# Performance work log

Hardware: AMD Instinct MI355X
Metric: run time of the kernel (lower is better)

## Reference

```python
import jax, jax.numpy as jnp
import numpy as np

NUM_HEADS = 4
NUM_GROUPS = 32
EPS = 1e-6


def group_norm(x, gamma, beta):
    # x: [b, c, h, w]
    b, c, h, w = x.shape
    xg = x.reshape(b, NUM_GROUPS, c // NUM_GROUPS, h, w)
    mu = xg.mean(axis=(2, 3, 4), keepdims=True)
    var = xg.var(axis=(2, 3, 4), keepdims=True)
    xn = ((xg - mu) * jax.lax.rsqrt(var + EPS)).reshape(b, c, h, w)
    return xn * gamma[None, :, None, None] + beta[None, :, None, None]


def conv1x1(x, W, b):
    # 1x1 conv == per-pixel channel matmul. W: [out_c, in_c], b: [out_c]
    return jnp.einsum('bchw,oc->bohw', x, W) + b[None, :, None, None]


def setup_inputs() -> dict:
    key = jax.random.key(0)
    ks = jax.random.split(key, 8)
    c = 256
    b, h, w = 1, 64, 64
    s = 1.0 / np.sqrt(c)
    return {
        'x_kv': jax.random.normal(ks[0], (b, c, h, w), dtype=jnp.float32),
        'gn_gamma': jnp.ones((c,), dtype=jnp.float32),
        'gn_beta': jnp.zeros((c,), dtype=jnp.float32),
        'Wq': jax.random.normal(ks[1], (c, c), dtype=jnp.float32) * s,
        'bq': jnp.zeros((c,), dtype=jnp.float32),
        'Wk': jax.random.normal(ks[2], (c, c), dtype=jnp.float32) * s,
        'bk': jnp.zeros((c,), dtype=jnp.float32),
        'Wv': jax.random.normal(ks[3], (c, c), dtype=jnp.float32) * s,
        'bv': jnp.zeros((c,), dtype=jnp.float32),
        'Wp': jax.random.normal(ks[4], (c, c), dtype=jnp.float32) * s,
        'bp': jnp.zeros((c,), dtype=jnp.float32),
    }


def reference(x_kv, gn_gamma, gn_beta, Wq, bq, Wk, bk, Wv, bv, Wp, bp):
    b, c, h, w = x_kv.shape
    hd = c // NUM_HEADS
    n = h * w

    h_norm = group_norm(x_kv, gn_gamma, gn_beta)  # self-attn: same norm for q,k,v

    q = conv1x1(h_norm, Wq, bq).reshape(b, NUM_HEADS, hd, n).transpose(0, 1, 3, 2)  # [b,H,n,hd]
    k = conv1x1(h_norm, Wk, bk).reshape(b, NUM_HEADS, hd, n)                        # [b,H,hd,n]
    v = conv1x1(h_norm, Wv, bv).reshape(b, NUM_HEADS, hd, n).transpose(0, 1, 3, 2)  # [b,H,n,hd]

    scores = jnp.einsum('bhnd,bhdm->bhnm', q, k) * (hd ** -0.5)  # [b,H,n,n]
    attn = jax.nn.softmax(scores, axis=-1)
    out = jnp.einsum('bhnm,bhmd->bhnd', attn, v)  # [b,H,n,hd]

    # Faithful to torch: permute(0,2,1,3).contiguous().view(b,c,h,w)
    out = out.transpose(0, 2, 1, 3).reshape(b, c, h, w)
    return x_kv + conv1x1(out, Wp, bp)
```

## Files before the change

### kernel.cpp

```cpp
#include <hip/hip_runtime.h>
#include <hip/hip_bf16.h>

#define NPIX 4096
#define CCH  256
#define HD   64
#define GSIZE 32768

#define QSCALE 0.18033688f

typedef __bf16 bf16x8 __attribute__((ext_vector_type(8)));
typedef __bf16 bf16x4 __attribute__((ext_vector_type(4)));
typedef __bf16 bf16x2 __attribute__((ext_vector_type(2)));
typedef float  f32x4  __attribute__((ext_vector_type(4)));
typedef unsigned int uint32x4 __attribute__((ext_vector_type(4)));

#define XPITCH 264

#if __has_builtin(__builtin_amdgcn_exp2f)
#define EXP2(x) __builtin_amdgcn_exp2f(x)
#else
#define EXP2(x) __expf((x) * 0.6931471805599453f)
#endif


__device__ __forceinline__ unsigned pack_bf16x2(float lo, float hi)
{
    bf16x2 v;
    v[0] = (__bf16)lo;
    v[1] = (__bf16)hi;
    return __builtin_bit_cast(unsigned, v);
}

__global__ __launch_bounds__(256) void stats_wconv(
    const float* __restrict__ X,
    const float* __restrict__ Wq, const float* __restrict__ Wk,
    const float* __restrict__ Wv, const float* __restrict__ Wp,
    float* __restrict__ psum, float* __restrict__ pssq, __bf16* __restrict__ Wb)
{
    const int bid = blockIdx.x, t = threadIdx.x;
    if (bid < 256) {
        const float* base = X + bid * 4096;
        float sum = 0.f, ssq = 0.f;
        #pragma unroll
        for (int k = 0; k < 4; ++k) {
            float4 v = *(const float4*)(base + t * 4 + k * 1024);
            sum += v.x + v.y + v.z + v.w;
            ssq += v.x * v.x + v.y * v.y + v.z * v.z + v.w * v.w;
        }
        #pragma unroll
        for (int off = 1; off < 64; off <<= 1) {
            sum += __shfl_xor(sum, off);
            ssq += __shfl_xor(ssq, off);
        }
        __shared__ float red[2][4];
        const int wv = t >> 6;
        if ((t & 63) == 0) { red[0][wv] = sum; red[1][wv] = ssq; }
        __syncthreads();
        if (t == 0) {
            psum[bid] = red[0][0] + red[0][1] + red[0][2] + red[0][3];
            pssq[bid] = red[1][0] + red[1][1] + red[1][2] + red[1][3];
        }
    } else {
        const int j0 = (bid - 256) * 4096 + t * 16;
        const int m  = j0 >> 16;
        const float* W = (m == 0) ? Wq : (m == 1) ? Wk : (m == 2) ? Wv : Wp;
        const float sc = (m == 0) ? QSCALE : 1.f;
        const int off = j0 & 65535;
        #pragma unroll
        for (int k = 0; k < 4; ++k) {
            float4 v = *(const float4*)(W + off + k * 4);
            bf16x4 o;
            o[0] = (__bf16)(v.x * sc); o[1] = (__bf16)(v.y * sc);
            o[2] = (__bf16)(v.z * sc); o[3] = (__bf16)(v.w * sc);
            *(bf16x4*)(Wb + m * 65536 + off + k * 4) = o;
        }
    }
}

__global__ __launch_bounds__(256) void gn_qkv(
    const float* __restrict__ X, const float* __restrict__ gamma,
    const float* __restrict__ beta,
    const float* __restrict__ psum, const float* __restrict__ pssq,
    const __bf16* __restrict__ Wb,
    const float* __restrict__ bq, const float* __restrict__ bk,
    const float* __restrict__ bv,
    __bf16* __restrict__ Qb, __bf16* __restrict__ Kb, __bf16* __restrict__ Vb)
{
    __shared__ __bf16 tile[64 * XPITCH];
    __shared__ float al[256], bl[256];

    const int t = threadIdx.x, lane = t & 63, wave = t >> 6;
    const int l16 = lane & 15, quad = lane >> 4;
    const int p0 = blockIdx.x * 64;
    const int z = blockIdx.y >> 1, och = blockIdx.y & 1;

    {
        const int g = t >> 3;
        float s = 0.f, q = 0.f;
        #pragma unroll
        for (int j = 0; j < 8; ++j) { s += psum[g * 8 + j]; q += pssq[g * 8 + j]; }
        const float mu  = s * (1.f / GSIZE);
        const float var = q * (1.f / GSIZE) - mu * mu;
        const float a = gamma[t] * rsqrtf(var + 1e-6f);
        al[t] = a;
        bl[t] = beta[t] - mu * a;
    }
    __syncthreads();

    #pragma unroll 4
    for (int i = 0; i < 16; ++i) {
        const int c4 = wave * 64 + i * 4;
        f32x4 a4 = *(const f32x4*)(al + c4);
        f32x4 b4 = *(const f32x4*)(bl + c4);
        bf16x4 pk;
        pk[0] = (__bf16)(X[(c4 + 0) * NPIX + p0 + lane] * a4[0] + b4[0]);
        pk[1] = (__bf16)(X[(c4 + 1) * NPIX + p0 + lane] * a4[1] + b4[1]);
        pk[2] = (__bf16)(X[(c4 + 2) * NPIX + p0 + lane] * a4[2] + b4[2]);
        pk[3] = (__bf16)(X[(c4 + 3) * NPIX + p0 + lane] * a4[3] + b4[3]);
        *(bf16x4*)(tile + lane * XPITCH + c4) = pk;
    }
    __syncthreads();

    const int pw = wave * 16;
    bf16x8 xf[8];
    #pragma unroll
    for (int kc = 0; kc < 8; ++kc)
        xf[kc] = *(const bf16x8*)(tile + (pw + l16) * XPITCH + kc * 32 + quad * 8);

    const __bf16* Wz = Wb + z * 65536;
    const float* bias = (z == 0) ? bq : (z == 1) ? bk : bv;

    if (z < 2) {
        const float qs = (z == 0) ? QSCALE : 1.f;
        __bf16* dst = (z == 0) ? Qb : Kb;
        #pragma unroll
        for (int grp = 0; grp < 2; ++grp) {
            f32x4 acc[4] = {};
            #pragma unroll
            for (int kc = 0; kc < 8; ++kc) {
                #pragma unroll
                for (int u = 0; u < 4; ++u) {
                    bf16x8 wf = *(const bf16x8*)(Wz + (och * 128 + (grp * 4 + u) * 16 + l16) * CCH + kc * 32 + quad * 8);
                    acc[u] = __builtin_amdgcn_mfma_f32_16x16x32_bf16(wf, xf[kc], acc[u], 0, 0, 0);
                }
            }
            #pragma unroll
            for (int u = 0; u < 4; ++u) {
                const int ot = och * 8 + grp * 4 + u;
                f32x4 bz = *(const f32x4*)(bias + och * 128 + (grp * 4 + u) * 16 + quad * 4);
                bf16x4 o;
                o[0] = (__bf16)(acc[u][0] + bz[0] * qs);
                o[1] = (__bf16)(acc[u][1] + bz[1] * qs);
                o[2] = (__bf16)(acc[u][2] + bz[2] * qs);
                o[3] = (__bf16)(acc[u][3] + bz[3] * qs);
                const int head = ot >> 2, dloc = (ot & 3) * 16 + quad * 4;
                *(bf16x4*)(dst + head * (NPIX * HD) + (p0 + pw + l16) * HD + dloc) = o;
            }
        }
    } else {
        #pragma unroll
        for (int grp = 0; grp < 2; ++grp) {
            f32x4 acc[4] = {};
            #pragma unroll
            for (int kc = 0; kc < 8; ++kc) {
                #pragma unroll
                for (int u = 0; u < 4; ++u) {
                    bf16x8 wf = *(const bf16x8*)(Wz + (och * 128 + (grp * 4 + u) * 16 + l16) * CCH + kc * 32 + quad * 8);
                    acc[u] = __builtin_amdgcn_mfma_f32_16x16x32_bf16(xf[kc], wf, acc[u], 0, 0, 0);
                }
            }
            #pragma unroll
            for (int u = 0; u < 4; ++u) {
                const int oc = och * 128 + (grp * 4 + u) * 16 + l16;
                const float bz = bias[oc];
                bf16x4 o;
                o[0] = (__bf16)(acc[u][0] + bz); o[1] = (__bf16)(acc[u][1] + bz);
                o[2] = (__bf16)(acc[u][2] + bz); o[3] = (__bf16)(acc[u][3] + bz);
                *(bf16x4*)(Vb + oc * NPIX + p0 + pw + quad * 4) = o;
            }
        }
    }
}

__global__ __launch_bounds__(256, 1) void attn_mfma(
    const __bf16* __restrict__ Qb, const __bf16* __restrict__ Kb,
    const __bf16* __restrict__ Vb, __bf16* __restrict__ Sb)
{
    __shared__ __align__(16) float co[4 * 64 * 68];
    __shared__ float cl[4 * 64];

    const int t = threadIdx.x, lane = t & 63, wave = t >> 6;
    const int l16 = lane & 15, quad = lane >> 4;

    const int bid  = blockIdx.x;
    const int head = (bid & 7) >> 1;
    const int qt   = ((bid >> 3) << 1) | (bid & 1);
    const int p0   = qt * 64;

    const __bf16* Qh = Qb + head * (NPIX * HD);
    const __bf16* Kh = Kb + head * (NPIX * HD) + (wave * 32 + l16) * HD + quad * 8;
    const __bf16* Vh = Vb + head * (HD * NPIX) + l16 * NPIX + wave * 32 + quad * 8;

    bf16x8 qf[4][2];
    #pragma unroll
    for (int rt = 0; rt < 4; ++rt) {
        const __bf16* qp = Qh + (p0 + rt * 16 + l16) * HD + quad * 8;
        qf[rt][0] = *(const bf16x8*)(qp);
        qf[rt][1] = *(const bf16x8*)(qp + 32);
    }

    bf16x8 ones;
    #pragma unroll
    for (int j = 0; j < 8; ++j) ones[j] = (__bf16)1.0f;

    f32x4 l_acc[4] = {};
    f32x4 o_acc[4][4] = {};

    auto ldKV = [&](int it,
                    bf16x8& k0, bf16x8& k1, bf16x8& k2, bf16x8& k3,
                    bf16x8& v0, bf16x8& v1, bf16x8& v2, bf16x8& v3) {
        const __bf16* kp = Kh + it * (128 * HD);
        k0 = *(const bf16x8*)(kp);
        k1 = *(const bf16x8*)(kp + 32);
        k2 = *(const bf16x8*)(kp + 16 * HD);
        k3 = *(const bf16x8*)(kp + 16 * HD + 32);
        const __bf16* vp = Vh + it * 128;
        v0 = *(const bf16x8*)(vp);
        v1 = *(const bf16x8*)(vp + 16 * NPIX);
        v2 = *(const bf16x8*)(vp + 32 * NPIX);
        v3 = *(const bf16x8*)(vp + 48 * NPIX);
    };

    auto step = [&](bf16x8 k0, bf16x8 k1, bf16x8 k2, bf16x8 k3,
                    bf16x8 v0, bf16x8 v1, bf16x8 v2, bf16x8 v3) {
        f32x4 st0[4] = {}, st1[4] = {};
        #pragma unroll
        for (int rt = 0; rt < 4; ++rt) {
            st0[rt] = __builtin_amdgcn_mfma_f32_16x16x32_bf16(k0, qf[rt][0], st0[rt], 0, 0, 0);
            st0[rt] = __builtin_amdgcn_mfma_f32_16x16x32_bf16(k1, qf[rt][1], st0[rt], 0, 0, 0);
            st1[rt] = __builtin_amdgcn_mfma_f32_16x16x32_bf16(k2, qf[rt][0], st1[rt], 0, 0, 0);
            st1[rt] = __builtin_amdgcn_mfma_f32_16x16x32_bf16(k3, qf[rt][1], st1[rt], 0, 0, 0);
        }
        #pragma unroll
        for (int rt = 0; rt < 4; ++rt) {
            unsigned a0 = pack_bf16x2(EXP2(st0[rt][0]), EXP2(st0[rt][1]));
            unsigned a1 = pack_bf16x2(EXP2(st0[rt][2]), EXP2(st0[rt][3]));
            unsigned b0 = pack_bf16x2(EXP2(st1[rt][0]), EXP2(st1[rt][1]));
            unsigned b1 = pack_bf16x2(EXP2(st1[rt][2]), EXP2(st1[rt][3]));
            asm("v_permlane32_swap_b32 %0, %1" : "+v"(a0), "+v"(b0));
            asm("v_permlane32_swap_b32 %0, %1" : "+v"(a1), "+v"(b1));
            asm("v_permlane16_swap_b32 %0, %1" : "+v"(a0), "+v"(b0));
            asm("v_permlane16_swap_b32 %0, %1" : "+v"(a1), "+v"(b1));
            uint32x4 w;
            w[0] = a0; w[1] = a1; w[2] = b0; w[3] = b1;
            const bf16x8 bp = __builtin_bit_cast(bf16x8, w);
            l_acc[rt] = __builtin_amdgcn_mfma_f32_16x16x32_bf16(ones, bp, l_acc[rt], 0, 0, 0);
            o_acc[0][rt] = __builtin_amdgcn_mfma_f32_16x16x32_bf16(v0, bp, o_acc[0][rt], 0, 0, 0);
            o_acc[1][rt] = __builtin_amdgcn_mfma_f32_16x16x32_bf16(v1, bp, o_acc[1][rt], 0, 0, 0);
            o_acc[2][rt] = __builtin_amdgcn_mfma_f32_16x16x32_bf16(v2, bp, o_acc[2][rt], 0, 0, 0);
            o_acc[3][rt] = __builtin_amdgcn_mfma_f32_16x16x32_bf16(v3, bp, o_acc[3][rt], 0, 0, 0);
        }
    };

    bf16x8 ka0, ka1, ka2, ka3, va0, va1, va2, va3;
    bf16x8 kb0, kb1, kb2, kb3, vb0, vb1, vb2, vb3;
    bf16x8 kc0, kc1, kc2, kc3, vc0, vc1, vc2, vc3;

    ldKV(0, ka0, ka1, ka2, ka3, va0, va1, va2, va3);
    ldKV(1, kb0, kb1, kb2, kb3, vb0, vb1, vb2, vb3);

    #pragma unroll 1
    for (int it = 0; it < 30; it += 3) {
        ldKV(it + 2, kc0, kc1, kc2, kc3, vc0, vc1, vc2, vc3);
        step(ka0, ka1, ka2, ka3, va0, va1, va2, va3);
        ldKV(it + 3, ka0, ka1, ka2, ka3, va0, va1, va2, va3);
        step(kb0, kb1, kb2, kb3, vb0, vb1, vb2, vb3);
        ldKV(it + 4, kb0, kb1, kb2, kb3, vb0, vb1, vb2, vb3);
        step(kc0, kc1, kc2, kc3, vc0, vc1, vc2, vc3);
    }
    step(ka0, ka1, ka2, ka3, va0, va1, va2, va3);
    step(kb0, kb1, kb2, kb3, vb0, vb1, vb2, vb3);

    #pragma unroll
    for (int dt = 0; dt < 4; ++dt)
        #pragma unroll
        for (int rt = 0; rt < 4; ++rt)
            *(f32x4*)(co + wave * 4352 + (rt * 16 + l16) * 68 + dt * 16 + quad * 4) = o_acc[dt][rt];
    if (quad == 0) {
        #pragma unroll
        for (int rt = 0; rt < 4; ++rt)
            cl[wave * 64 + rt * 16 + l16] = l_acc[rt][0];
    }
    __syncthreads();

    {
        const int row = t >> 2, dc = (t & 3) * 16;
        const float l = cl[row] + cl[64 + row] + cl[128 + row] + cl[192 + row];
        const float inv = 1.f / l;
        f32x4 s[4];
        #pragma unroll
        for (int j = 0; j < 4; ++j) {
            s[j] = f32x4{0.f, 0.f, 0.f, 0.f};
            #pragma unroll
            for (int w = 0; w < 4; ++w)
                s[j] += *(const f32x4*)(co + w * 4352 + row * 68 + dc + j * 4);
        }
        bf16x8 o1, o2;
        #pragma unroll
        for (int j = 0; j < 4; ++j) {
            o1[j]     = (__bf16)(s[0][j] * inv);
            o1[j + 4] = (__bf16)(s[1][j] * inv);
            o2[j]     = (__bf16)(s[2][j] * inv);
            o2[j + 4] = (__bf16)(s[3][j] * inv);
        }
        __bf16* dst = Sb + (p0 + row) * CCH + head * HD + dc;
        *(bf16x8*)(dst)     = o1;
        *(bf16x8*)(dst + 8) = o2;
    }
}

__global__ __launch_bounds__(256) void gemm_proj(
    const __bf16* __restrict__ Sb, const __bf16* __restrict__ Wpb,
    const float* __restrict__ bias, const float* __restrict__ X,
    float* __restrict__ Out)
{
    __shared__ __bf16 Bs[32 * XPITCH];

    const int t = threadIdx.x, lane = t & 63, wave = t >> 6;
    const int l16 = lane & 15, quad = lane >> 4;
    const int p0  = blockIdx.x * 32;
    const int och = blockIdx.y;

    #pragma unroll
    for (int pg = 0; pg < 4; ++pg) {
        bf16x8 v = *(const bf16x8*)(Sb + t * NPIX + p0 + pg * 8);
        #pragma unroll
        for (int j = 0; j < 8; ++j)
            Bs[(pg * 8 + j) * XPITCH + t] = v[j];
    }
    __syncthreads();

    const int pixset = wave & 1, ocset = wave >> 1;
    bf16x8 af[8];
    #pragma unroll
    for (int kc = 0; kc < 8; ++kc)
        af[kc] = *(const bf16x8*)(Bs + (pixset * 16 + l16) * XPITCH + kc * 32 + quad * 8);

    #pragma unroll
    for (int u = 0; u < 4; ++u) {
        f32x4 acc = {};
        const int oc_t = och * 128 + ocset * 64 + u * 16;
        #pragma unroll
        for (int kc = 0; kc < 8; ++kc) {
            bf16x8 wf = *(const bf16x8*)(Wpb + (oc_t + l16) * CCH + kc * 32 + quad * 8);
            acc = __builtin_amdgcn_mfma_f32_16x16x32_bf16(af[kc], wf, acc, 0, 0, 0);
        }
        const int oc  = oc_t + l16;
        const int pix = p0 + pixset * 16 + quad * 4;
        const float bz = bias[oc];
        f32x4 r4 = *(const f32x4*)(X + oc * NPIX + pix);
        f32x4 y;
        y[0] = acc[0] + bz + r4[0];
        y[1] = acc[1] + bz + r4[1];
        y[2] = acc[2] + bz + r4[2];
        y[3] = acc[3] + bz + r4[3];
        *(f32x4*)(Out + oc * NPIX + pix) = y;
    }
}

extern "C" void kernel_launch(void* const* d_in, const int* in_sizes, int n_in,
                              void* d_out, int out_size, void* d_ws, size_t ws_size,
                              hipStream_t stream)
{
    const float* x     = (const float*)d_in[0];
    const float* gamma = (const float*)d_in[1];
    const float* beta  = (const float*)d_in[2];
    const float* Wq    = (const float*)d_in[3];
    const float* bq    = (const float*)d_in[4];
    const float* Wk    = (const float*)d_in[5];
    const float* bk    = (const float*)d_in[6];
    const float* Wv    = (const float*)d_in[7];
    const float* bv    = (const float*)d_in[8];
    const float* Wp    = (const float*)d_in[9];
    const float* bp    = (const float*)d_in[10];
    float* out = (float*)d_out;

    char* ws = (char*)d_ws;
    float*  psum = (float*)(ws);
    float*  pssq = (float*)(ws + 1024);
    __bf16* Wb   = (__bf16*)(ws + 65536);
    __bf16* Qb   = (__bf16*)(ws + (1 << 20));
    __bf16* Kb   = (__bf16*)(ws + (3 << 20));
    __bf16* Vb   = (__bf16*)(ws + (5 << 20));
    __bf16* Sb   = (__bf16*)(ws + (7 << 20));

    stats_wconv<<<320, 256, 0, stream>>>(x, Wq, Wk, Wv, Wp, psum, pssq, Wb);

    dim3 gq(64, 6);
    gn_qkv<<<gq, 256, 0, stream>>>(x, gamma, beta, psum, pssq, Wb,
                                   bq, bk, bv, Qb, Kb, Vb);

    attn_mfma<<<256, 256, 0, stream>>>(Qb, Kb, Vb, Sb);

    dim3 gp(128, 2);
    gemm_proj<<<gp, 256, 0, stream>>>(Sb, Wb + 3 * 65536, bp, x, out);
}
```

Baseline: 140.9 us.

## Split attention over key halves with 128-row query tiles, merge in projection

The attention kernel now processes 128 query rows per block instead of 64, and each block covers only half of the keys. It writes unnormalized fp32 partial outputs and row sums to workspace. The projection GEMM then sums the two halves and normalizes them while staging its input. This doubles K/V reuse per load and keeps the grid at 256 blocks, at the cost of more registers, a larger LDS footprint, and extra fp32 partial traffic through global memory.

```diff
diff --git a/kernel.cpp b/kernel.cpp
--- a/kernel.cpp
+++ b/kernel.cpp
@@ -182,28 +182,31 @@
     }
 }
 
-__global__ __launch_bounds__(256, 1) void attn_mfma(
+__global__ __launch_bounds__(256, 1) void attn_partial(
     const __bf16* __restrict__ Qb, const __bf16* __restrict__ Kb,
-    const __bf16* __restrict__ Vb, __bf16* __restrict__ Sb)
-{
-    __shared__ __align__(16) float co[4 * 64 * 68];
-    __shared__ float cl[4 * 64];
+    const __bf16* __restrict__ Vb, float* __restrict__ Op,
+    float* __restrict__ Lp)
+{
+    __shared__ __align__(16) float co[4 * 128 * 68];
+    __shared__ float cl[4 * 128];
 
     const int t = threadIdx.x, lane = t & 63, wave = t >> 6;
     const int l16 = lane & 15, quad = lane >> 4;
 
     const int bid  = blockIdx.x;
     const int head = (bid & 7) >> 1;
-    const int qt   = ((bid >> 3) << 1) | (bid & 1);
-    const int p0   = qt * 64;
+    const int half = bid & 1;
+    const int qt   = bid >> 3;
+    const int p0   = qt * 128;
+    const int kt0  = half * 16;
 
     const __bf16* Qh = Qb + head * (NPIX * HD);
     const __bf16* Kh = Kb + head * (NPIX * HD) + (wave * 32 + l16) * HD + quad * 8;
     const __bf16* Vh = Vb + head * (HD * NPIX) + l16 * NPIX + wave * 32 + quad * 8;
 
-    bf16x8 qf[4][2];
-    #pragma unroll
-    for (int rt = 0; rt < 4; ++rt) {
+    bf16x8 qf[8][2];
+    #pragma unroll
+    for (int rt = 0; rt < 8; ++rt) {
         const __bf16* qp = Qh + (p0 + rt * 16 + l16) * HD + quad * 8;
         qf[rt][0] = *(const bf16x8*)(qp);
         qf[rt][1] = *(const bf16x8*)(qp + 32);
@@ -213,8 +216,8 @@
     #pragma unroll
     for (int j = 0; j < 8; ++j) ones[j] = (__bf16)1.0f;
 
-    f32x4 l_acc[4] = {};
-    f32x4 o_acc[4][4] = {};
+    f32x4 l_acc[8] = {};
+    f32x4 o_acc[4][8] = {};
 
     auto ldKV = [&](int it,
                     bf16x8& k0, bf16x8& k1, bf16x8& k2, bf16x8& k3,
@@ -233,94 +236,89 @@
 
     auto step = [&](bf16x8 k0, bf16x8 k1, bf16x8 k2, bf16x8 k3,
                     bf16x8 v0, bf16x8 v1, bf16x8 v2, bf16x8 v3) {
-        f32x4 st0[4] = {}, st1[4] = {};
-        #pragma unroll
-        for (int rt = 0; rt < 4; ++rt) {
-            st0[rt] = __builtin_amdgcn_mfma_f32_16x16x32_bf16(k0, qf[rt][0], st0[rt], 0, 0, 0);
-            st0[rt] = __builtin_amdgcn_mfma_f32_16x16x32_bf16(k1, qf[rt][1], st0[rt], 0, 0, 0);
-            st1[rt] = __builtin_amdgcn_mfma_f32_16x16x32_bf16(k2, qf[rt][0], st1[rt], 0, 0, 0);
-            st1[rt] = __builtin_amdgcn_mfma_f32_16x16x32_bf16(k3, qf[rt][1], st1[rt], 0, 0, 0);
-        }
-        #pragma unroll
-        for (int rt = 0; rt < 4; ++rt) {
-            unsigned a0 = pack_bf16x2(EXP2(st0[rt][0]), EXP2(st0[rt][1]));
-            unsigned a1 = pack_bf16x2(EXP2(st0[rt][2]), EXP2(st0[rt][3]));
-            unsigned b0 = pack_bf16x2(EXP2(st1[rt][0]), EXP2(st1[rt][1]));
-            unsigned b1 = pack_bf16x2(EXP2(st1[rt][2]), EXP2(st1[rt][3]));
-            asm("v_permlane32_swap_b32 %0, %1" : "+v"(a0), "+v"(b0));
-            asm("v_permlane32_swap_b32 %0, %1" : "+v"(a1), "+v"(b1));
-            asm("v_permlane16_swap_b32 %0, %1" : "+v"(a0), "+v"(b0));
-            asm("v_permlane16_swap_b32 %0, %1" : "+v"(a1), "+v"(b1));
-            uint32x4 w;
-            w[0] = a0; w[1] = a1; w[2] = b0; w[3] = b1;
-            const bf16x8 bp = __builtin_bit_cast(bf16x8, w);
-            l_acc[rt] = __builtin_amdgcn_mfma_f32_16x16x32_bf16(ones, bp, l_acc[rt], 0, 0, 0);
-            o_acc[0][rt] = __builtin_amdgcn_mfma_f32_16x16x32_bf16(v0, bp, o_acc[0][rt], 0, 0, 0);
-            o_acc[1][rt] = __builtin_amdgcn_mfma_f32_16x16x32_bf16(v1, bp, o_acc[1][rt], 0, 0, 0);
-            o_acc[2][rt] = __builtin_amdgcn_mfma_f32_16x16x32_bf16(v2, bp, o_acc[2][rt], 0, 0, 0);
-            o_acc[3][rt] = __builtin_amdgcn_mfma_f32_16x16x32_bf16(v3, bp, o_acc[3][rt], 0, 0, 0);
+        #pragma unroll
+        for (int rtb = 0; rtb < 2; ++rtb) {
+            f32x4 st0[4] = {}, st1[4] = {};
+            #pragma unroll
+            for (int rt = 0; rt < 4; ++rt) {
+                const int r = rtb * 4 + rt;
+                st0[rt] = __builtin_amdgcn_mfma_f32_16x16x32_bf16(k0, qf[r][0], st0[rt], 0, 0, 0);
+                st0[rt] = __builtin_amdgcn_mfma_f32_16x16x32_bf16(k1, qf[r][1], st0[rt], 0, 0, 0);
+                st1[rt] = __builtin_amdgcn_mfma_f32_16x16x32_bf16(k2, qf[r][0], st1[rt], 0, 0, 0);
+                st1[rt] = __builtin_amdgcn_mfma_f32_16x16x32_bf16(k3, qf[r][1], st1[rt], 0, 0, 0);
+            }
+            #pragma unroll
+            for (int rt = 0; rt < 4; ++rt) {
+                const int r = rtb * 4 + rt;
+                unsigned a0 = pack_bf16x2(EXP2(st0[rt][0]), EXP2(st0[rt][1]));
+                unsigned a1 = pack_bf16x2(EXP2(st0[rt][2]), EXP2(st0[rt][3]));
+                unsigned b0 = pack_bf16x2(EXP2(st1[rt][0]), EXP2(st1[rt][1]));
+                unsigned b1 = pack_bf16x2(EXP2(st1[rt][2]), EXP2(st1[rt][3]));
+                asm("v_permlane32_swap_b32 %0, %1" : "+v"(a0), "+v"(b0));
+                asm("v_permlane32_swap_b32 %0, %1" : "+v"(a1), "+v"(b1));
+                asm("v_permlane16_swap_b32 %0, %1" : "+v"(a0), "+v"(b0));
+                asm("v_permlane16_swap_b32 %0, %1" : "+v"(a1), "+v"(b1));
+                uint32x4 w;
+                w[0] = a0; w[1] = a1; w[2] = b0; w[3] = b1;
+                const bf16x8 bp = __builtin_bit_cast(bf16x8, w);
+                l_acc[r] = __builtin_amdgcn_mfma_f32_16x16x32_bf16(ones, bp, l_acc[r], 0, 0, 0);
+                o_acc[0][r] = __builtin_amdgcn_mfma_f32_16x16x32_bf16(v0, bp, o_acc[0][r], 0, 0, 0);
+                o_acc[1][r] = __builtin_amdgcn_mfma_f32_16x16x32_bf16(v1, bp, o_acc[1][r], 0, 0, 0);
+                o_acc[2][r] = __builtin_amdgcn_mfma_f32_16x16x32_bf16(v2, bp, o_acc[2][r], 0, 0, 0);
+                o_acc[3][r] = __builtin_amdgcn_mfma_f32_16x16x32_bf16(v3, bp, o_acc[3][r], 0, 0, 0);
+            }
         }
     };
 
     bf16x8 ka0, ka1, ka2, ka3, va0, va1, va2, va3;
     bf16x8 kb0, kb1, kb2, kb3, vb0, vb1, vb2, vb3;
-    bf16x8 kc0, kc1, kc2, kc3, vc0, vc1, vc2, vc3;
-
-    ldKV(0, ka0, ka1, ka2, ka3, va0, va1, va2, va3);
-    ldKV(1, kb0, kb1, kb2, kb3, vb0, vb1, vb2, vb3);
-
+
+    ldKV(kt0, ka0, ka1, ka2, ka3, va0, va1, va2, va3);
     #pragma unroll 1
-    for (int it = 0; it < 30; it += 3) {
-        ldKV(it + 2, kc0, kc1, kc2, kc3, vc0, vc1, vc2, vc3);
+    for (int it = 0; it < 16; it += 2) {
+        ldKV(kt0 + it + 1, kb0, kb1, kb2, kb3, vb0, vb1, vb2, vb3);
         step(ka0, ka1, ka2, ka3, va0, va1, va2, va3);
-        ldKV(it + 3, ka0, ka1, ka2, ka3, va0, va1, va2, va3);
+        if (it + 2 < 16)
+            ldKV(kt0 + it + 2, ka0, ka1, ka2, ka3, va0, va1, va2, va3);
         step(kb0, kb1, kb2, kb3, vb0, vb1, vb2, vb3);
-        ldKV(it + 4, kb0, kb1, kb2, kb3, vb0, vb1, vb2, vb3);
-        step(kc0, kc1, kc2, kc3, vc0, vc1, vc2, vc3);
-    }
-    step(ka0, ka1, ka2, ka3, va0, va1, va2, va3);
-    step(kb0, kb1, kb2, kb3, vb0, vb1, vb2, vb3);
+    }
 
     #pragma unroll
     for (int dt = 0; dt < 4; ++dt)
         #pragma unroll
-        for (int rt = 0; rt < 4; ++rt)
-            *(f32x4*)(co + wave * 4352 + (rt * 16 + l16) * 68 + dt * 16 + quad * 4) = o_acc[dt][rt];
+        for (int rt = 0; rt < 8; ++rt)
+            *(f32x4*)(co + wave * 8704 + (rt * 16 + l16) * 68 + dt * 16 + quad * 4) = o_acc[dt][rt];
     if (quad == 0) {
         #pragma unroll
-        for (int rt = 0; rt < 4; ++rt)
-            cl[wave * 64 + rt * 16 + l16] = l_acc[rt][0];
+        for (int rt = 0; rt < 8; ++rt)
+            cl[wave * 128 + rt * 16 + l16] = l_acc[rt][0];
     }
     __syncthreads();
 
     {
-        const int row = t >> 2, dc = (t & 3) * 16;
-        const float l = cl[row] + cl[64 + row] + cl[128 + row] + cl[192 + row];
-        const float inv = 1.f / l;
-        f32x4 s[4];
-        #pragma unroll
-        for (int j = 0; j < 4; ++j) {
+        const int row = t >> 1, dhalf = t & 1, dc = dhalf * 32;
+        f32x4 s[8];
+        #pragma unroll
+        for (int j = 0; j < 8; ++j) {
             s[j] = f32x4{0.f, 0.f, 0.f, 0.f};
             #pragma unroll
             for (int w = 0; w < 4; ++w)
-                s[j] += *(const f32x4*)(co + w * 4352 + row * 68 + dc + j * 4);
-        }
-        bf16x8 o1, o2;
-        #pragma unroll
-        for (int j = 0; j < 4; ++j) {
-            o1[j]     = (__bf16)(s[0][j] * inv);
-            o1[j + 4] = (__bf16)(s[1][j] * inv);
-            o2[j]     = (__bf16)(s[2][j] * inv);
-            o2[j + 4] = (__bf16)(s[3][j] * inv);
-        }
-        __bf16* dst = Sb + (p0 + row) * CCH + head * HD + dc;
-        *(bf16x8*)(dst)     = o1;
-        *(bf16x8*)(dst + 8) = o2;
+                s[j] += *(const f32x4*)(co + w * 8704 + row * 68 + dc + j * 4);
+        }
+        float* dsto = Op + half * (NPIX * CCH) + (p0 + row) * CCH + head * HD + dc;
+        #pragma unroll
+        for (int j = 0; j < 8; ++j)
+            *(f32x4*)(dsto + j * 4) = s[j];
+        if (dhalf == 0) {
+            const float l = cl[row] + cl[128 + row] + cl[256 + row] + cl[384 + row];
+            Lp[half * 16384 + head * 4096 + p0 + row] = l;
+        }
     }
 }
 
 __global__ __launch_bounds__(256) void gemm_proj(
-    const __bf16* __restrict__ Sb, const __bf16* __restrict__ Wpb,
+    const float* __restrict__ Op, const float* __restrict__ Lp,
+    const __bf16* __restrict__ Wpb,
     const float* __restrict__ bias, const float* __restrict__ X,
     float* __restrict__ Out)
 {
@@ -333,10 +331,21 @@
 
     #pragma unroll
     for (int pg = 0; pg < 4; ++pg) {
-        bf16x8 v = *(const bf16x8*)(Sb + t * NPIX + p0 + pg * 8);
-        #pragma unroll
-        for (int j = 0; j < 8; ++j)
-            Bs[(pg * 8 + j) * XPITCH + t] = v[j];
+        const int col  = p0 + pg * 8;
+        const int gidx = t * NPIX + col;
+        const int P    = gidx >> 8;
+        const int hd8  = (gidx >> 6) & 3;
+        const float l  = Lp[hd8 * 4096 + P] + Lp[16384 + hd8 * 4096 + P];
+        const float inv = 1.f / l;
+        f32x4 a0 = *(const f32x4*)(Op + gidx);
+        f32x4 a1 = *(const f32x4*)(Op + gidx + 4);
+        f32x4 b0 = *(const f32x4*)(Op + NPIX * CCH + gidx);
+        f32x4 b1 = *(const f32x4*)(Op + NPIX * CCH + gidx + 4);
+        #pragma unroll
+        for (int j = 0; j < 4; ++j) {
+            Bs[(pg * 8 + j) * XPITCH + t]       = (__bf16)((a0[j] + b0[j]) * inv);
+            Bs[(pg * 8 + j + 4) * XPITCH + t]   = (__bf16)((a1[j] + b1[j]) * inv);
+        }
     }
     __syncthreads();
 
@@ -392,7 +401,8 @@
     __bf16* Qb   = (__bf16*)(ws + (1 << 20));
     __bf16* Kb   = (__bf16*)(ws + (3 << 20));
     __bf16* Vb   = (__bf16*)(ws + (5 << 20));
-    __bf16* Sb   = (__bf16*)(ws + (7 << 20));
+    float*  Op   = (float*)(ws + (16 << 20));
+    float*  Lp   = (float*)(ws + (25 << 20));
 
     stats_wconv<<<320, 256, 0, stream>>>(x, Wq, Wk, Wv, Wp, psum, pssq, Wb);
 
@@ -400,8 +410,8 @@
     gn_qkv<<<gq, 256, 0, stream>>>(x, gamma, beta, psum, pssq, Wb,
                                    bq, bk, bv, Qb, Kb, Vb);
 
-    attn_mfma<<<256, 256, 0, stream>>>(Qb, Kb, Vb, Sb);
+    attn_partial<<<256, 256, 0, stream>>>(Qb, Kb, Vb, Op, Lp);
 
     dim3 gp(128, 2);
-    gemm_proj<<<gp, 256, 0, stream>>>(Sb, Wb + 3 * 65536, bp, x, out);
-}
+    gemm_proj<<<gp, 256, 0, stream>>>(Op, Lp, Wb + 3 * 65536, bp, x, out);
+}
```

Result: no change. 142.5 us (+1.2%).

## Software-pipeline QK, exp and PV stages across key tiles in attention loop

Applied to the files above, without the earlier changes.

Splits the per-tile attention step into separate QK-matmul, exp/pack, and PV-matmul stages and interleaves them across two tiles, so the QK MFMAs of the next tile overlap the exp work of the current one. K and V loads are issued separately and later, reducing the buffer set from three to two. The extra score arrays raise register pressure, and clamped indices at the tail cause a few redundant loads and an extra QK for the last iteration.

```diff
diff --git a/kernel.cpp b/kernel.cpp
--- a/kernel.cpp
+++ b/kernel.cpp
@@ -216,70 +216,83 @@
     f32x4 l_acc[4] = {};
     f32x4 o_acc[4][4] = {};
 
-    auto ldKV = [&](int it,
-                    bf16x8& k0, bf16x8& k1, bf16x8& k2, bf16x8& k3,
-                    bf16x8& v0, bf16x8& v1, bf16x8& v2, bf16x8& v3) {
+    bf16x8 kA0, kA1, kA2, kA3, vA0, vA1, vA2, vA3;
+    bf16x8 kB0, kB1, kB2, kB3, vB0, vB1, vB2, vB3;
+    f32x4 sA0[4], sA1[4], sB0[4], sB1[4];
+    bf16x8 bp[4];
+
+    auto ldK = [&](int it, bf16x8& k0, bf16x8& k1, bf16x8& k2, bf16x8& k3) {
         const __bf16* kp = Kh + it * (128 * HD);
         k0 = *(const bf16x8*)(kp);
         k1 = *(const bf16x8*)(kp + 32);
         k2 = *(const bf16x8*)(kp + 16 * HD);
         k3 = *(const bf16x8*)(kp + 16 * HD + 32);
+    };
+    auto ldV = [&](int it, bf16x8& v0, bf16x8& v1, bf16x8& v2, bf16x8& v3) {
         const __bf16* vp = Vh + it * 128;
         v0 = *(const bf16x8*)(vp);
         v1 = *(const bf16x8*)(vp + 16 * NPIX);
         v2 = *(const bf16x8*)(vp + 32 * NPIX);
         v3 = *(const bf16x8*)(vp + 48 * NPIX);
     };
-
-    auto step = [&](bf16x8 k0, bf16x8 k1, bf16x8 k2, bf16x8 k3,
-                    bf16x8 v0, bf16x8 v1, bf16x8 v2, bf16x8 v3) {
-        f32x4 st0[4] = {}, st1[4] = {};
+    auto qk = [&](bf16x8 k0, bf16x8 k1, bf16x8 k2, bf16x8 k3,
+                  f32x4 (&s0)[4], f32x4 (&s1)[4]) {
         #pragma unroll
         for (int rt = 0; rt < 4; ++rt) {
-            st0[rt] = __builtin_amdgcn_mfma_f32_16x16x32_bf16(k0, qf[rt][0], st0[rt], 0, 0, 0);
-            st0[rt] = __builtin_amdgcn_mfma_f32_16x16x32_bf16(k1, qf[rt][1], st0[rt], 0, 0, 0);
-            st1[rt] = __builtin_amdgcn_mfma_f32_16x16x32_bf16(k2, qf[rt][0], st1[rt], 0, 0, 0);
-            st1[rt] = __builtin_amdgcn_mfma_f32_16x16x32_bf16(k3, qf[rt][1], st1[rt], 0, 0, 0);
-        }
+            f32x4 z = {0.f, 0.f, 0.f, 0.f};
+            s0[rt] = __builtin_amdgcn_mfma_f32_16x16x32_bf16(k0, qf[rt][0], z, 0, 0, 0);
+            s0[rt] = __builtin_amdgcn_mfma_f32_16x16x32_bf16(k1, qf[rt][1], s0[rt], 0, 0, 0);
+            s1[rt] = __builtin_amdgcn_mfma_f32_16x16x32_bf16(k2, qf[rt][0], z, 0, 0, 0);
+            s1[rt] = __builtin_amdgcn_mfma_f32_16x16x32_bf16(k3, qf[rt][1], s1[rt], 0, 0, 0);
+        }
+    };
+    auto exppack = [&](const f32x4 (&s0)[4], const f32x4 (&s1)[4]) {
         #pragma unroll
         for (int rt = 0; rt < 4; ++rt) {
-            unsigned a0 = pack_bf16x2(EXP2(st0[rt][0]), EXP2(st0[rt][1]));
-            unsigned a1 = pack_bf16x2(EXP2(st0[rt][2]), EXP2(st0[rt][3]));
-            unsigned b0 = pack_bf16x2(EXP2(st1[rt][0]), EXP2(st1[rt][1]));
-            unsigned b1 = pack_bf16x2(EXP2(st1[rt][2]), EXP2(st1[rt][3]));
+            unsigned a0 = pack_bf16x2(EXP2(s0[rt][0]), EXP2(s0[rt][1]));
+            unsigned a1 = pack_bf16x2(EXP2(s0[rt][2]), EXP2(s0[rt][3]));
+            unsigned b0 = pack_bf16x2(EXP2(s1[rt][0]), EXP2(s1[rt][1]));
+            unsigned b1 = pack_bf16x2(EXP2(s1[rt][2]), EXP2(s1[rt][3]));
             asm("v_permlane32_swap_b32 %0, %1" : "+v"(a0), "+v"(b0));
             asm("v_permlane32_swap_b32 %0, %1" : "+v"(a1), "+v"(b1));
             asm("v_permlane16_swap_b32 %0, %1" : "+v"(a0), "+v"(b0));
             asm("v_permlane16_swap_b32 %0, %1" : "+v"(a1), "+v"(b1));
             uint32x4 w;
             w[0] = a0; w[1] = a1; w[2] = b0; w[3] = b1;
-            const bf16x8 bp = __builtin_bit_cast(bf16x8, w);
-            l_acc[rt] = __builtin_amdgcn_mfma_f32_16x16x32_bf16(ones, bp, l_acc[rt], 0, 0, 0);
-            o_acc[0][rt] = __builtin_amdgcn_mfma_f32_16x16x32_bf16(v0, bp, o_acc[0][rt], 0, 0, 0);
-            o_acc[1][rt] = __builtin_amdgcn_mfma_f32_16x16x32_bf16(v1, bp, o_acc[1][rt], 0, 0, 0);
-            o_acc[2][rt] = __builtin_amdgcn_mfma_f32_16x16x32_bf16(v2, bp, o_acc[2][rt], 0, 0, 0);
-            o_acc[3][rt] = __builtin_amdgcn_mfma_f32_16x16x32_bf16(v3, bp, o_acc[3][rt], 0, 0, 0);
+            bp[rt] = __builtin_bit_cast(bf16x8, w);
         }
     };
-
-    bf16x8 ka0, ka1, ka2, ka3, va0, va1, va2, va3;
-    bf16x8 kb0, kb1, kb2, kb3, vb0, vb1, vb2, vb3;
-    bf16x8 kc0, kc1, kc2, kc3, vc0, vc1, vc2, vc3;
-
-    ldKV(0, ka0, ka1, ka2, ka3, va0, va1, va2, va3);
-    ldKV(1, kb0, kb1, kb2, kb3, vb0, vb1, vb2, vb3);
+    auto pv = [&](bf16x8 v0, bf16x8 v1, bf16x8 v2, bf16x8 v3) {
+        #pragma unroll
+        for (int rt = 0; rt < 4; ++rt) {
+            l_acc[rt] = __builtin_amdgcn_mfma_f32_16x16x32_bf16(ones, bp[rt], l_acc[rt], 0, 0, 0);
+            o_acc[0][rt] = __builtin_amdgcn_mfma_f32_16x16x32_bf16(v0, bp[rt], o_acc[0][rt], 0, 0, 0);
+            o_acc[1][rt] = __builtin_amdgcn_mfma_f32_16x16x32_bf16(v1, bp[rt], o_acc[1][rt], 0, 0, 0);
+            o_acc[2][rt] = __builtin_amdgcn_mfma_f32_16x16x32_bf16(v2, bp[rt], o_acc[2][rt], 0, 0, 0);
+            o_acc[3][rt] = __builtin_amdgcn_mfma_f32_16x16x32_bf16(v3, bp[rt], o_acc[3][rt], 0, 0, 0);
+        }
+    };
+
+    ldK(0, kA0, kA1, kA2, kA3);  ldV(0, vA0, vA1, vA2, vA3);
+    ldK(1, kB0, kB1, kB2, kB3);  ldV(1, vB0, vB1, vB2, vB3);
+    qk(kA0, kA1, kA2, kA3, sA0, sA1);
 
     #pragma unroll 1
-    for (int it = 0; it < 30; it += 3) {
-        ldKV(it + 2, kc0, kc1, kc2, kc3, vc0, vc1, vc2, vc3);
-        step(ka0, ka1, ka2, ka3, va0, va1, va2, va3);
-        ldKV(it + 3, ka0, ka1, ka2, ka3, va0, va1, va2, va3);
-        step(kb0, kb1, kb2, kb3, vb0, vb1, vb2, vb3);
-        ldKV(it + 4, kb0, kb1, kb2, kb3, vb0, vb1, vb2, vb3);
-        step(kc0, kc1, kc2, kc3, vc0, vc1, vc2, vc3);
-    }
-    step(ka0, ka1, ka2, ka3, va0, va1, va2, va3);
-    step(kb0, kb1, kb2, kb3, vb0, vb1, vb2, vb3);
+    for (int it = 0; it < 32; it += 2) {
+        const int n2 = (it + 2 < 32) ? it + 2 : 31;
+        const int n3 = (it + 3 < 32) ? it + 3 : 31;
+
+        qk(kB0, kB1, kB2, kB3, sB0, sB1);
+        ldK(n2, kA0, kA1, kA2, kA3);
+        exppack(sA0, sA1);
+        pv(vA0, vA1, vA2, vA3);
+        ldV(n2, vA0, vA1, vA2, vA3);
+        exppack(sB0, sB1);
+        qk(kA0, kA1, kA2, kA3, sA0, sA1);
+        pv(vB0, vB1, vB2, vB3);
+        ldK(n3, kB0, kB1, kB2, kB3);
+        ldV(n3, vB0, vB1, vB2, vB3);
+    }
 
     #pragma unroll
     for (int dt = 0; dt < 4; ++dt)
```

New measurement: 143.6 us. Within noise of the previous version (+1.9%).

## Switch attention kernel to 32x32x16 MFMA tiles with VALU row-sum

Applied to the files above, without the earlier changes.

Reworks the attention inner loop to use 32x32x16 bf16 MFMA instructions instead of 16x16x32, which changes the register layout of Q, K, V and the output accumulators. The softmax denominator is now summed on the VALU from the exponentials and combined across half-waves with a permlane swap, rather than computed with an extra MFMA against a ones vector. The K/V prefetch pipeline drops from triple to double buffering. Larger MFMA tiles mean fewer instruction issues and less operand traffic, at the cost of longer per-instruction latency and less prefetch depth.

```diff
diff --git a/kernel.cpp b/kernel.cpp
--- a/kernel.cpp
+++ b/kernel.cpp
@@ -12,6 +12,7 @@
 typedef __bf16 bf16x4 __attribute__((ext_vector_type(4)));
 typedef __bf16 bf16x2 __attribute__((ext_vector_type(2)));
 typedef float  f32x4  __attribute__((ext_vector_type(4)));
+typedef float  f32x16 __attribute__((ext_vector_type(16)));
 typedef unsigned int uint32x4 __attribute__((ext_vector_type(4)));
 
 #define XPITCH 264
@@ -190,107 +191,125 @@
     __shared__ float cl[4 * 64];
 
     const int t = threadIdx.x, lane = t & 63, wave = t >> 6;
-    const int l16 = lane & 15, quad = lane >> 4;
+    const int c31 = lane & 31, hi = lane >> 5;
 
     const int bid  = blockIdx.x;
     const int head = (bid & 7) >> 1;
     const int qt   = ((bid >> 3) << 1) | (bid & 1);
     const int p0   = qt * 64;
 
+    const __bf16* Kl = Kb + head * (NPIX * HD) + (wave * 32 + c31) * HD + hi * 8;
+    const __bf16* Vl = Vb + (head * HD + c31) * NPIX + wave * 32 + hi * 8;
     const __bf16* Qh = Qb + head * (NPIX * HD);
-    const __bf16* Kh = Kb + head * (NPIX * HD) + (wave * 32 + l16) * HD + quad * 8;
-    const __bf16* Vh = Vb + head * (HD * NPIX) + l16 * NPIX + wave * 32 + quad * 8;
-
-    bf16x8 qf[4][2];
-    #pragma unroll
-    for (int rt = 0; rt < 4; ++rt) {
-        const __bf16* qp = Qh + (p0 + rt * 16 + l16) * HD + quad * 8;
-        qf[rt][0] = *(const bf16x8*)(qp);
-        qf[rt][1] = *(const bf16x8*)(qp + 32);
-    }
-
-    bf16x8 ones;
-    #pragma unroll
-    for (int j = 0; j < 8; ++j) ones[j] = (__bf16)1.0f;
-
-    f32x4 l_acc[4] = {};
-    f32x4 o_acc[4][4] = {};
+
+    bf16x8 qf[2][4];
+    #pragma unroll
+    for (int nt = 0; nt < 2; ++nt)
+        #pragma unroll
+        for (int c = 0; c < 4; ++c)
+            qf[nt][c] = *(const bf16x8*)(Qh + (p0 + nt * 32 + c31) * HD + c * 16 + hi * 8);
+
+    f32x16 o_acc[2][2] = {};
+    float l_run[2] = {0.f, 0.f};
 
     auto ldKV = [&](int it,
                     bf16x8& k0, bf16x8& k1, bf16x8& k2, bf16x8& k3,
                     bf16x8& v0, bf16x8& v1, bf16x8& v2, bf16x8& v3) {
-        const __bf16* kp = Kh + it * (128 * HD);
+        const __bf16* kp = Kl + it * (128 * HD);
         k0 = *(const bf16x8*)(kp);
-        k1 = *(const bf16x8*)(kp + 32);
-        k2 = *(const bf16x8*)(kp + 16 * HD);
-        k3 = *(const bf16x8*)(kp + 16 * HD + 32);
-        const __bf16* vp = Vh + it * 128;
+        k1 = *(const bf16x8*)(kp + 16);
+        k2 = *(const bf16x8*)(kp + 32);
+        k3 = *(const bf16x8*)(kp + 48);
+        const __bf16* vp = Vl + it * 128;
         v0 = *(const bf16x8*)(vp);
-        v1 = *(const bf16x8*)(vp + 16 * NPIX);
+        v1 = *(const bf16x8*)(vp + 16);
         v2 = *(const bf16x8*)(vp + 32 * NPIX);
-        v3 = *(const bf16x8*)(vp + 48 * NPIX);
+        v3 = *(const bf16x8*)(vp + 32 * NPIX + 16);
+    };
+
+    auto procP = [&](const f32x16& st, float& lrun, bf16x8& bc0, bf16x8& bc1) {
+        float pf[16];
+        #pragma unroll
+        for (int r = 0; r < 16; ++r) pf[r] = EXP2(st[r]);
+        lrun += (((pf[0] + pf[1]) + (pf[2] + pf[3])) + ((pf[4] + pf[5]) + (pf[6] + pf[7])))
+              + (((pf[8] + pf[9]) + (pf[10] + pf[11])) + ((pf[12] + pf[13]) + (pf[14] + pf[15])));
+        unsigned x0 = pack_bf16x2(pf[0], pf[1]);
+        unsigned x1 = pack_bf16x2(pf[2], pf[3]);
+        unsigned x2 = pack_bf16x2(pf[4], pf[5]);
+        unsigned x3 = pack_bf16x2(pf[6], pf[7]);
+        asm("v_permlane32_swap_b32 %0, %1" : "+v"(x0), "+v"(x2));
+        asm("v_permlane32_swap_b32 %0, %1" : "+v"(x1), "+v"(x3));
+        uint32x4 w0; w0[0] = x0; w0[1] = x1; w0[2] = x2; w0[3] = x3;
+        bc0 = __builtin_bit_cast(bf16x8, w0);
+        unsigned x4 = pack_bf16x2(pf[8], pf[9]);
+        unsigned x5 = pack_bf16x2(pf[10], pf[11]);
+        unsigned x6 = pack_bf16x2(pf[12], pf[13]);
+        unsigned x7 = pack_bf16x2(pf[14], pf[15]);
+        asm("v_permlane32_swap_b32 %0, %1" : "+v"(x4), "+v"(x6));
+        asm("v_permlane32_swap_b32 %0, %1" : "+v"(x5), "+v"(x7));
+        uint32x4 w1; w1[0] = x4; w1[1] = x5; w1[2] = x6; w1[3] = x7;
+        bc1 = __builtin_bit_cast(bf16x8, w1);
     };
 
     auto step = [&](bf16x8 k0, bf16x8 k1, bf16x8 k2, bf16x8 k3,
                     bf16x8 v0, bf16x8 v1, bf16x8 v2, bf16x8 v3) {
-        f32x4 st0[4] = {}, st1[4] = {};
-        #pragma unroll
-        for (int rt = 0; rt < 4; ++rt) {
-            st0[rt] = __builtin_amdgcn_mfma_f32_16x16x32_bf16(k0, qf[rt][0], st0[rt], 0, 0, 0);
-            st0[rt] = __builtin_amdgcn_mfma_f32_16x16x32_bf16(k1, qf[rt][1], st0[rt], 0, 0, 0);
-            st1[rt] = __builtin_amdgcn_mfma_f32_16x16x32_bf16(k2, qf[rt][0], st1[rt], 0, 0, 0);
-            st1[rt] = __builtin_amdgcn_mfma_f32_16x16x32_bf16(k3, qf[rt][1], st1[rt], 0, 0, 0);
-        }
-        #pragma unroll
-        for (int rt = 0; rt < 4; ++rt) {
-            unsigned a0 = pack_bf16x2(EXP2(st0[rt][0]), EXP2(st0[rt][1]));
-            unsigned a1 = pack_bf16x2(EXP2(st0[rt][2]), EXP2(st0[rt][3]));
-            unsigned b0 = pack_bf16x2(EXP2(st1[rt][0]), EXP2(st1[rt][1]));
-            unsigned b1 = pack_bf16x2(EXP2(st1[rt][2]), EXP2(st1[rt][3]));
-            asm("v_permlane32_swap_b32 %0, %1" : "+v"(a0), "+v"(b0));
-            asm("v_permlane32_swap_b32 %0, %1" : "+v"(a1), "+v"(b1));
-            asm("v_permlane16_swap_b32 %0, %1" : "+v"(a0), "+v"(b0));
-            asm("v_permlane16_swap_b32 %0, %1" : "+v"(a1), "+v"(b1));
-            uint32x4 w;
-            w[0] = a0; w[1] = a1; w[2] = b0; w[3] = b1;
-            const bf16x8 bp = __builtin_bit_cast(bf16x8, w);
-            l_acc[rt] = __builtin_amdgcn_mfma_f32_16x16x32_bf16(ones, bp, l_acc[rt], 0, 0, 0);
-            o_acc[0][rt] = __builtin_amdgcn_mfma_f32_16x16x32_bf16(v0, bp, o_acc[0][rt], 0, 0, 0);
-            o_acc[1][rt] = __builtin_amdgcn_mfma_f32_16x16x32_bf16(v1, bp, o_acc[1][rt], 0, 0, 0);
-            o_acc[2][rt] = __builtin_amdgcn_mfma_f32_16x16x32_bf16(v2, bp, o_acc[2][rt], 0, 0, 0);
-            o_acc[3][rt] = __builtin_amdgcn_mfma_f32_16x16x32_bf16(v3, bp, o_acc[3][rt], 0, 0, 0);
-        }
+        f32x16 st0 = {}, st1 = {};
+        st0 = __builtin_amdgcn_mfma_f32_32x32x16_bf16(k0, qf[0][0], st0, 0, 0, 0);
+        st1 = __builtin_amdgcn_mfma_f32_32x32x16_bf16(k0, qf[1][0], st1, 0, 0, 0);
+        st0 = __builtin_amdgcn_mfma_f32_32x32x16_bf16(k1, qf[0][1], st0, 0, 0, 0);
+        st1 = __builtin_amdgcn_mfma_f32_32x32x16_bf16(k1, qf[1][1], st1, 0, 0, 0);
+        st0 = __builtin_amdgcn_mfma_f32_32x32x16_bf16(k2, qf[0][2], st0, 0, 0, 0);
+        st1 = __builtin_amdgcn_mfma_f32_32x32x16_bf16(k2, qf[1][2], st1, 0, 0, 0);
+        st0 = __builtin_amdgcn_mfma_f32_32x32x16_bf16(k3, qf[0][3], st0, 0, 0, 0);
+        st1 = __builtin_amdgcn_mfma_f32_32x32x16_bf16(k3, qf[1][3], st1, 0, 0, 0);
+
+        bf16x8 b00, b01, b10, b11;
+        procP(st0, l_run[0], b00, b01);
+        procP(st1, l_run[1], b10, b11);
+
+        o_acc[0][0] = __builtin_amdgcn_mfma_f32_32x32x16_bf16(v0, b00, o_acc[0][0], 0, 0, 0);
+        o_acc[0][1] = __builtin_amdgcn_mfma_f32_32x32x16_bf16(v0, b10, o_acc[0][1], 0, 0, 0);
+        o_acc[1][0] = __builtin_amdgcn_mfma_f32_32x32x16_bf16(v2, b00, o_acc[1][0], 0, 0, 0);
+        o_acc[1][1] = __builtin_amdgcn_mfma_f32_32x32x16_bf16(v2, b10, o_acc[1][1], 0, 0, 0);
+        o_acc[0][0] = __builtin_amdgcn_mfma_f32_32x32x16_bf16(v1, b01, o_acc[0][0], 0, 0, 0);
+        o_acc[0][1] = __builtin_amdgcn_mfma_f32_32x32x16_bf16(v1, b11, o_acc[0][1], 0, 0, 0);
+        o_acc[1][0] = __builtin_amdgcn_mfma_f32_32x32x16_bf16(v3, b01, o_acc[1][0], 0, 0, 0);
+        o_acc[1][1] = __builtin_amdgcn_mfma_f32_32x32x16_bf16(v3, b11, o_acc[1][1], 0, 0, 0);
     };
 
     bf16x8 ka0, ka1, ka2, ka3, va0, va1, va2, va3;
     bf16x8 kb0, kb1, kb2, kb3, vb0, vb1, vb2, vb3;
-    bf16x8 kc0, kc1, kc2, kc3, vc0, vc1, vc2, vc3;
-
     ldKV(0, ka0, ka1, ka2, ka3, va0, va1, va2, va3);
-    ldKV(1, kb0, kb1, kb2, kb3, vb0, vb1, vb2, vb3);
-
     #pragma unroll 1
-    for (int it = 0; it < 30; it += 3) {
-        ldKV(it + 2, kc0, kc1, kc2, kc3, vc0, vc1, vc2, vc3);
+    for (int it = 0; it < 32; it += 2) {
+        ldKV(it + 1, kb0, kb1, kb2, kb3, vb0, vb1, vb2, vb3);
         step(ka0, ka1, ka2, ka3, va0, va1, va2, va3);
-        ldKV(it + 3, ka0, ka1, ka2, ka3, va0, va1, va2, va3);
+        if (it + 2 < 32)
+            ldKV(it + 2, ka0, ka1, ka2, ka3, va0, va1, va2, va3);
         step(kb0, kb1, kb2, kb3, vb0, vb1, vb2, vb3);
-        ldKV(it + 4, kb0, kb1, kb2, kb3, vb0, vb1, vb2, vb3);
-        step(kc0, kc1, kc2, kc3, vc0, vc1, vc2, vc3);
-    }
-    step(ka0, ka1, ka2, ka3, va0, va1, va2, va3);
-    step(kb0, kb1, kb2, kb3, vb0, vb1, vb2, vb3);
-
-    #pragma unroll
-    for (int dt = 0; dt < 4; ++dt)
-        #pragma unroll
-        for (int rt = 0; rt < 4; ++rt)
-            *(f32x4*)(co + wave * 4352 + (rt * 16 + l16) * 68 + dt * 16 + quad * 4) = o_acc[dt][rt];
-    if (quad == 0) {
-        #pragma unroll
-        for (int rt = 0; rt < 4; ++rt)
-            cl[wave * 64 + rt * 16 + l16] = l_acc[rt][0];
-    }
+    }
+
+    {
+        unsigned u0 = __builtin_bit_cast(unsigned, l_run[0]);
+        unsigned u1 = __builtin_bit_cast(unsigned, l_run[1]);
+        asm("v_permlane32_swap_b32 %0, %1" : "+v"(u0), "+v"(u1));
+        const float lfin = __builtin_bit_cast(float, u0) + __builtin_bit_cast(float, u1);
+        cl[wave * 64 + hi * 32 + c31] = lfin;
+    }
+
+    #pragma unroll
+    for (int dt = 0; dt < 2; ++dt)
+        #pragma unroll
+        for (int nt = 0; nt < 2; ++nt)
+            #pragma unroll
+            for (int g = 0; g < 4; ++g) {
+                f32x4 v;
+                v[0] = o_acc[dt][nt][g * 4 + 0];
+                v[1] = o_acc[dt][nt][g * 4 + 1];
+                v[2] = o_acc[dt][nt][g * 4 + 2];
+                v[3] = o_acc[dt][nt][g * 4 + 3];
+                *(f32x4*)(co + wave * 4352 + (nt * 32 + c31) * 68 + dt * 32 + g * 8 + hi * 4) = v;
+            }
     __syncthreads();
 
     {
```

Result: no change. 142.9 us (+1.4%).
